# Optimization experiments

Hardware: AMD Instinct MI355X
Metric: run time of the kernel (lower is better)

## Reference

```python
import jax, jax.numpy as jnp
import numpy as np

TAPS, DIMS, SPS = 32, 2, 2
LR_W, LR_F, LR_S, LR_B = 1.0 / 2**6, 1.0 / 2**7, 0.0, 1.0 / 2**11
GRAD_MAX_W, GRAD_MAX_F = 30.0, 30.0
EPS, BETA = 1e-8, 0.0


def _const16qam():
    # commplax comm.const('16QAM', norm=True): unit-average-power 16QAM grid
    p = np.array([-3.0, -1.0, 1.0, 3.0], dtype=np.float32)
    c = (p[:, None] + 1j * p[None, :]).reshape(-1) / np.sqrt(10.0)
    return jnp.asarray(c, dtype=jnp.complex64)


def _frame(x, flen, fstep):
    # xop.frame: [L, D] -> [(L-flen)//fstep + 1, flen, D]
    n = (x.shape[0] - flen) // fstep + 1
    idx = jnp.arange(n)[:, None] * fstep + jnp.arange(flen)[None, :]
    return x[idx]


def _clip(g, gmax):
    # same math as jnp.where(|g|>gmax, g/|g|*gmax, g), but NaN-safe under AD
    ag = jnp.abs(g)
    return g * jnp.minimum(1.0, gmax / jnp.maximum(ag, 1e-30))


def _ddlms(x):
    const = _const16qam()
    u_all = _frame(x, TAPS, SPS)  # [N, taps, dims] complex64

    def step(state, u):
        w, f, s, b, fshat = state
        v = jnp.einsum('ijt,tj->i', w, u)          # mimo filter output [dims]
        k = v * f
        c = k * s
        z = c + b
        q = v * fshat + b
        # decision-directed symbol (train=False, no truth)
        d = const[jnp.argmin(jnp.abs(const[:, None] - q[None, :]), axis=0)]
        psi_hat = jnp.abs(f) / f * jnp.abs(s) / s
        e_w = (d - b) * psi_hat - v
        e_f = d - b - k
        e_s = d - b - c
        e_b = d - z
        gw = -1.0 / ((jnp.abs(u) ** 2).sum() + EPS) * e_w[:, None, None] * u.conj().T[None, ...]
        gf = -1.0 / (jnp.abs(v) ** 2 + EPS) * e_f * v.conj()
        gs = -1.0 / (jnp.abs(k) ** 2 + EPS) * e_s * k.conj()
        gb = -e_b
        gw = _clip(gw, GRAD_MAX_W)
        gf = _clip(gf, GRAD_MAX_F)
        out = (w, f, s, b)  # pre-update params are used by apply
        wn = w - LR_W * gw
        fn = f - LR_F * gf
        sn = s - LR_S * gs
        bn = b - LR_B * gb
        fshatn = BETA * fshat + (1.0 - BETA) * (fn * sn)
        return (wn, fn, sn, bn, fshatn), out

    dt = jnp.complex64
    state0 = (jnp.zeros((DIMS, DIMS, TAPS), dt),   # w0 (mimoinit='zeros')
              jnp.ones((DIMS,), dt),               # f0
              jnp.ones((DIMS,), dt),               # s0
              jnp.zeros((DIMS,), dt),              # b0
              jnp.ones((DIMS,), dt))               # fshat0
    _, (ws, fs, ss, bs) = jax.lax.scan(step, state0, u_all)
    # mimo_apply: vmap(mimo)(ws, u_all) * fs * ss + bs
    y = jnp.einsum('nijt,ntj->ni', ws, u_all) * fs * ss + bs  # [N, dims]
    return y


def setup_inputs() -> dict:
    key = jax.random.key(0)
    k1, k2 = jax.random.split(key)
    x_re = jax.random.normal(k1, (200000, 2), dtype=jnp.float32)
    x_im = jax.random.normal(k2, (200000, 2), dtype=jnp.float32)
    return {"x_re": x_re, "x_im": x_im}


def reference(x_re, x_im):
    x = jax.lax.complex(x_re, x_im)  # [2N, 2] complex64
    y = _ddlms(x)                    # [(2N-taps)//sps + 1, 2] complex64
    return jnp.stack([y.real, y.imag], axis=-1)  # [N_out, 2, 2] float32
```

## Files before the change

kernel.cpp:

```cpp
#include <hip/hip_runtime.h>

typedef unsigned u2v __attribute__((ext_vector_type(2)));

template<int CTRL>
__device__ __forceinline__ float dpp_xadd(float v) {
    int s = __builtin_amdgcn_update_dpp(0, __float_as_int(v), CTRL, 0xF, 0xF, true);
    return v + __int_as_float(s);
}

#if __has_builtin(__builtin_amdgcn_permlane16_swap)
__device__ __forceinline__ float xor16_add(float v) {
    u2v r = __builtin_amdgcn_permlane16_swap((unsigned)__float_as_int(v),
                                             (unsigned)__float_as_int(v),
                                             false, false);
    return __int_as_float((int)r.x) + __int_as_float((int)r.y);
}
#else
__device__ __forceinline__ float xor16_add(float v) {
    int s = __builtin_amdgcn_ds_swizzle(__float_as_int(v), 0x401F);
    return v + __int_as_float(s);
}
#endif

__device__ __forceinline__ float red32(float v) {
    v = dpp_xadd<0xB1>(v);
    v = dpp_xadd<0x4E>(v);
    v = dpp_xadd<0x141>(v);
    v = dpp_xadd<0x140>(v);
    v = xor16_add(v);
    return v;
}

__global__ void pre_tab(const float* __restrict__ xre,
                        const float* __restrict__ xim,
                        float4* __restrict__ tab, int ns) {
    int n = blockIdx.x * blockDim.x + threadIdx.x;
    if (n >= ns) return;
    const float* ar = xre + 4 * n;
    const float* ai = xim + 4 * n;
    float un = 0.f;
    #pragma unroll 8
    for (int k = 0; k < 64; ++k) un = fmaf(ar[k], ar[k], fmaf(ai[k], ai[k], un));
    float s = (1.0f / 64.0f) / (un + 1e-8f);
    float cr = 0.f, ci = 0.f;
    if (n + 1 < ns) {
        const float* br_ = ar + 4;
        const float* bi_ = ai + 4;
        #pragma unroll 8
        for (int k = 0; k < 64; ++k) {
            cr = fmaf(ar[k], br_[k], fmaf(ai[k], bi_[k], cr));
            ci = fmaf(ar[k], bi_[k], ci);
            ci = fmaf(-ai[k], br_[k], ci);
        }
    }
    tab[n] = make_float4(s, s * cr, s * ci, 0.f);
}

template<bool PRE>
__global__ __launch_bounds__(64, 1)
void ddlms_scan(const float* __restrict__ xre,
                const float* __restrict__ xim,
                const float4* __restrict__ tab,
                float* __restrict__ out) {
    const int l = (int)threadIdx.x;
    const int m = l & 31;
    const int half = l >> 5;

    constexpr float EPSv = 1e-8f;
    constexpr float LRW  = 1.0f / 64.0f;
    constexpr float LRF  = 1.0f / 128.0f;
    constexpr float LRB  = 1.0f / 2048.0f;
    const float B1 = 0.6324555320336759f;
    const float A1 = 0.31622776601683794f;
    const float A3 = 0.9486832980505138f;

    float wAr=0.f, wAi=0.f, wBr=0.f, wBi=0.f;
    float fr=1.f, fi=0.f, br=0.f, bi=0.f;
    float psr=1.f, psj=0.f;
    float vr=0.f, vi=0.f;
    float ewPr=0.f, ewPi=0.f, sP=0.f;

    float2* __restrict__ o2 = reinterpret_cast<float2*>(out);
    const int NS = 99985;

    auto LOADU = [&](int nn, float& a, float& b_, float& c, float& d_) {
        const float* pr = xre + 4 * nn;
        const float* pi = xim + 4 * nn;
        a = pr[m]; c = pr[m + 32]; b_ = pi[m]; d_ = pi[m + 32];
    };
    auto LOADT = [&](int nn, float& s, float& cr, float& ci) {
        if constexpr (PRE) {
            float4 t = tab[nn];
            s = t.x; cr = t.y; ci = t.z;
        }
    };

    float u0Ar,u0Ai,u0Br,u0Bi, u1Ar,u1Ai,u1Br,u1Bi,
          u2Ar,u2Ai,u2Br,u2Bi, u3Ar,u3Ai,u3Br,u3Bi;
    float t0s=0,t0r=0,t0i=0, t1s=0,t1r=0,t1i=0,
          t2s=0,t2r=0,t2i=0, t3s=0,t3r=0,t3i=0;

    u3Ar=u3Ai=u3Br=u3Bi=0.f;
    LOADU(0, u0Ar,u0Ai,u0Br,u0Bi);
    LOADU(1, u1Ar,u1Ai,u1Br,u1Bi);
    LOADU(2, u2Ar,u2Ai,u2Br,u2Bi);
    LOADT(0, t0s,t0r,t0i);
    LOADT(1, t1s,t1r,t1i);
    LOADT(2, t2s,t2r,t2i);

    auto STEP = [&](int n,
        float& uPAr, float& uPAi, float& uPBr, float& uPBi,
        float& uCAr, float& uCAi, float& uCBr, float& uCBi,
        float& uNAr, float& uNAi, float& uNBr, float& uNBi,
        float& tCs, float& tCr, float& tCi,
        float& tFs, float& tFr, float& tFi) {

        {
            float gr = ewPr * uPAr; gr = fmaf( ewPi, uPAi, gr);
            float gi = ewPi * uPAr; gi = fmaf(-ewPr, uPAi, gi);
            wAr = fmaf(sP, gr, wAr); wAi = fmaf(sP, gi, wAi);
            float hr = ewPr * uPBr; hr = fmaf( ewPi, uPBi, hr);
            float hi = ewPi * uPBr; hi = fmaf(-ewPr, uPBi, hi);
            wBr = fmaf(sP, hr, wBr); wBi = fmaf(sP, hi, wBi);
        }

        {
            int nn = n + 3; if (nn > NS - 1) nn = NS - 1;
            LOADU(nn, uPAr, uPAi, uPBr, uPBi);
            LOADT(nn, tFs, tFr, tFi);
        }

        float basr, basi;
        {
            float prr = wAr * uNAr; prr = fmaf(-wAi, uNAi, prr);
            prr = fmaf(wBr, uNBr, prr); prr = fmaf(-wBi, uNBi, prr);
            float pri = wAr * uNAi; pri = fmaf( wAi, uNAr, pri);
            pri = fmaf(wBr, uNBi, pri); pri = fmaf( wBi, uNBr, pri);
            basr = red32(prr); basi = red32(pri);
        }

        float sN, sCr, sCi;
        if constexpr (PRE) {
            sN = tCs; sCr = tCr; sCi = tCi;
        } else {
            float uu = uCAr * uCAr; uu = fmaf(uCAi, uCAi, uu);
            uu = fmaf(uCBr, uCBr, uu); uu = fmaf(uCBi, uCBi, uu);
            sN = LRW * __builtin_amdgcn_rcpf(red32(uu) + EPSv);
            float ccr = uCAr * uNAr; ccr = fmaf(uCAi, uNAi, ccr);
            ccr = fmaf(uCBr, uNBr, ccr); ccr = fmaf(uCBi, uNBi, ccr);
            float cci = uCAr * uNAi; cci = fmaf(-uCAi, uNAr, cci);
            cci = fmaf(uCBr, uNBi, cci); cci = fmaf(-uCBi, uNBr, cci);
            sCr = sN * red32(ccr); sCi = sN * red32(cci);
        }

        float kr = fmaf(vr, fr, -(vi * fi));
        float ki = fmaf(vr, fi,   vi * fr);
        float zr = kr + br, zi = ki + bi;
        if (m == 0) o2[2 * n + half] = make_float2(zr, zi);

        float magr = (fabsf(zr) > B1) ? A3 : A1;
        float dr   = (zr <= 0.f) ? -magr : magr;
        float magi = (fabsf(zi) > B1) ? A3 : A1;
        float di   = (zi <= 0.f) ? -magi : magi;

        float er = dr - zr, ei = di - zi;

        float v2  = fmaf(vr, vr, fmaf(vi, vi, EPSv));
        float rv  = __builtin_amdgcn_rcpf(v2);
        float gfr = fmaf(er, vr,   ei * vi)  * rv;
        float gfi = fmaf(ei, vr, -(er * vi)) * rv;
        float m2  = fmaf(gfr, gfr, gfi * gfi);
        float scf = fminf(1.f, 30.f * __builtin_amdgcn_rsqf(m2));
        float tf  = LRF * scf;

        float dbr = dr - br, dbi = di - bi;
        float ewr = fmaf(dbr, psr, -(dbi * psj)) - vr;
        float ewi = fmaf(dbr, psj,   dbi * psr)  - vi;

        float Dr = fmaf(ewr, sCr, -(ewi * sCi));
        float Di = fmaf(ewr, sCi,   ewi * sCr);
        vr = basr + Dr;
        vi = basi + Di;

        fr = fmaf(tf, gfr, fr); fi = fmaf(tf, gfi, fi);
        br = fmaf(LRB, er, br); bi = fmaf(LRB, ei, bi);

        float ff = fmaf(fr, fr, fi * fi);
        float rs = __builtin_amdgcn_rsqf(ff);
        psr = fr * rs; psj = -(fi * rs);

        ewPr = ewr; ewPi = ewi; sP = sN;
    };

    int n = 0;
    for (int it = 0; it < 24996; ++it) {
        STEP(n+0, u3Ar,u3Ai,u3Br,u3Bi, u0Ar,u0Ai,u0Br,u0Bi,
                  u1Ar,u1Ai,u1Br,u1Bi, t0s,t0r,t0i, t3s,t3r,t3i);
        STEP(n+1, u0Ar,u0Ai,u0Br,u0Bi, u1Ar,u1Ai,u1Br,u1Bi,
                  u2Ar,u2Ai,u2Br,u2Bi, t1s,t1r,t1i, t0s,t0r,t0i);
        STEP(n+2, u1Ar,u1Ai,u1Br,u1Bi, u2Ar,u2Ai,u2Br,u2Bi,
                  u3Ar,u3Ai,u3Br,u3Bi, t2s,t2r,t2i, t1s,t1r,t1i);
        STEP(n+3, u2Ar,u2Ai,u2Br,u2Bi, u3Ar,u3Ai,u3Br,u3Bi,
                  u0Ar,u0Ai,u0Br,u0Bi, t3s,t3r,t3i, t2s,t2r,t2i);
        n += 4;
    }
    STEP(99984, u3Ar,u3Ai,u3Br,u3Bi, u0Ar,u0Ai,u0Br,u0Bi,
                u1Ar,u1Ai,u1Br,u1Bi, t0s,t0r,t0i, t3s,t3r,t3i);
}

extern "C" void kernel_launch(void* const* d_in, const int* in_sizes, int n_in,
                              void* d_out, int out_size, void* d_ws, size_t ws_size,
                              hipStream_t stream) {
    const float* xre = (const float*)d_in[0];
    const float* xim = (const float*)d_in[1];
    float* out = (float*)d_out;
    const int NS = 99985;

    if (ws_size >= (size_t)NS * sizeof(float4)) {
        float4* tab = (float4*)d_ws;
        pre_tab<<<(NS + 255) / 256, 256, 0, stream>>>(xre, xim, tab, NS);
        ddlms_scan<true><<<1, 64, 0, stream>>>(xre, xim, tab, out);
    } else {
        ddlms_scan<false><<<1, 64, 0, stream>>>(xre, xim, nullptr, out);
    }
}
```

Before: 21.67 ms.

## Batch output stores across 32 steps and use fused DPP adds in reductions

Each step no longer does a single-lane conditional store. Lane (n mod 32) latches z into a register, and after every 32 steps all lanes write one coalesced store. This takes a divergent branch and a global store out of the serial critical path of each step. The cross-lane reduction also now uses inline-asm v_add_f32 with DPP modifiers (quad_perm, half-mirror, mirror), folding the move and add into one instruction, though inline asm may limit compiler scheduling.

```diff
diff --git a/kernel.cpp b/kernel.cpp
--- a/kernel.cpp
+++ b/kernel.cpp
@@ -2,10 +2,21 @@
 
 typedef unsigned u2v __attribute__((ext_vector_type(2)));
 
-template<int CTRL>
-__device__ __forceinline__ float dpp_xadd(float v) {
-    int s = __builtin_amdgcn_update_dpp(0, __float_as_int(v), CTRL, 0xF, 0xF, true);
-    return v + __int_as_float(s);
+__device__ __forceinline__ float dppadd_x1(float v) {
+    float r; asm("v_add_f32 %0, %1, %1 quad_perm:[1,0,3,2] row_mask:0xf bank_mask:0xf"
+                 : "=v"(r) : "v"(v)); return r;
+}
+__device__ __forceinline__ float dppadd_x2(float v) {
+    float r; asm("v_add_f32 %0, %1, %1 quad_perm:[2,3,0,1] row_mask:0xf bank_mask:0xf"
+                 : "=v"(r) : "v"(v)); return r;
+}
+__device__ __forceinline__ float dppadd_x7(float v) {
+    float r; asm("v_add_f32 %0, %1, %1 row_half_mirror row_mask:0xf bank_mask:0xf"
+                 : "=v"(r) : "v"(v)); return r;
+}
+__device__ __forceinline__ float dppadd_x15(float v) {
+    float r; asm("v_add_f32 %0, %1, %1 row_mirror row_mask:0xf bank_mask:0xf"
+                 : "=v"(r) : "v"(v)); return r;
 }
 
 #if __has_builtin(__builtin_amdgcn_permlane16_swap)
@@ -23,10 +34,10 @@
 #endif
 
 __device__ __forceinline__ float red32(float v) {
-    v = dpp_xadd<0xB1>(v);
-    v = dpp_xadd<0x4E>(v);
-    v = dpp_xadd<0x141>(v);
-    v = dpp_xadd<0x140>(v);
+    v = dppadd_x1(v);
+    v = dppadd_x2(v);
+    v = dppadd_x7(v);
+    v = dppadd_x15(v);
     v = xor16_add(v);
     return v;
 }
@@ -79,6 +90,7 @@
     float psr=1.f, psj=0.f;
     float vr=0.f, vi=0.f;
     float ewPr=0.f, ewPi=0.f, sP=0.f;
+    float zsr=0.f, zsi=0.f;
 
     float2* __restrict__ o2 = reinterpret_cast<float2*>(out);
     const int NS = 99985;
@@ -156,7 +168,12 @@
         float kr = fmaf(vr, fr, -(vi * fi));
         float ki = fmaf(vr, fi,   vi * fr);
         float zr = kr + br, zi = ki + bi;
-        if (m == 0) o2[2 * n + half] = make_float2(zr, zi);
+
+        {
+            bool c = (m == (n & 31));
+            zsr = c ? zr : zsr;
+            zsi = c ? zi : zsi;
+        }
 
         float magr = (fabsf(zr) > B1) ? A3 : A1;
         float dr   = (zr <= 0.f) ? -magr : magr;
@@ -192,20 +209,31 @@
         ewPr = ewr; ewPi = ewi; sP = sN;
     };
 
+    #define STEP4()                                                        \
+        STEP(n+0, u3Ar,u3Ai,u3Br,u3Bi, u0Ar,u0Ai,u0Br,u0Bi,               \
+                  u1Ar,u1Ai,u1Br,u1Bi, t0s,t0r,t0i, t3s,t3r,t3i);         \
+        STEP(n+1, u0Ar,u0Ai,u0Br,u0Bi, u1Ar,u1Ai,u1Br,u1Bi,               \
+                  u2Ar,u2Ai,u2Br,u2Bi, t1s,t1r,t1i, t0s,t0r,t0i);         \
+        STEP(n+2, u1Ar,u1Ai,u1Br,u1Bi, u2Ar,u2Ai,u2Br,u2Bi,               \
+                  u3Ar,u3Ai,u3Br,u3Bi, t2s,t2r,t2i, t1s,t1r,t1i);         \
+        STEP(n+3, u2Ar,u2Ai,u2Br,u2Bi, u3Ar,u3Ai,u3Br,u3Bi,               \
+                  u0Ar,u0Ai,u0Br,u0Bi, t3s,t3r,t3i, t2s,t2r,t2i);         \
+        n += 4
+
     int n = 0;
-    for (int it = 0; it < 24996; ++it) {
-        STEP(n+0, u3Ar,u3Ai,u3Br,u3Bi, u0Ar,u0Ai,u0Br,u0Bi,
-                  u1Ar,u1Ai,u1Br,u1Bi, t0s,t0r,t0i, t3s,t3r,t3i);
-        STEP(n+1, u0Ar,u0Ai,u0Br,u0Bi, u1Ar,u1Ai,u1Br,u1Bi,
-                  u2Ar,u2Ai,u2Br,u2Bi, t1s,t1r,t1i, t0s,t0r,t0i);
-        STEP(n+2, u1Ar,u1Ai,u1Br,u1Bi, u2Ar,u2Ai,u2Br,u2Bi,
-                  u3Ar,u3Ai,u3Br,u3Bi, t2s,t2r,t2i, t1s,t1r,t1i);
-        STEP(n+3, u2Ar,u2Ai,u2Br,u2Bi, u3Ar,u3Ai,u3Br,u3Bi,
-                  u0Ar,u0Ai,u0Br,u0Bi, t3s,t3r,t3i, t2s,t2r,t2i);
-        n += 4;
-    }
+    for (int big = 0; big < 3124; ++big) {
+        for (int j8 = 0; j8 < 8; ++j8) { STEP4(); }
+        float2 val; val.x = zsr; val.y = zsi;
+        o2[2 * (n - 32 + m) + half] = val;
+    }
+    for (int j8 = 0; j8 < 4; ++j8) { STEP4(); }
     STEP(99984, u3Ar,u3Ai,u3Br,u3Bi, u0Ar,u0Ai,u0Br,u0Bi,
                 u1Ar,u1Ai,u1Br,u1Bi, t0s,t0r,t0i, t3s,t3r,t3i);
+    if (m <= 16) {
+        float2 val; val.x = zsr; val.y = zsi;
+        o2[2 * (99968 + m) + half] = val;
+    }
+    #undef STEP4
 }
 
 extern "C" void kernel_launch(void* const* d_in, const int* in_sizes, int n_in,
```

Measured after the change: 25.86 ms. +19.3%, slower.
